# Optimization experiments

Measured on AMD Instinct MI355X. Metric: run time of the kernel, lower is better.

The kernel has to match this reference:

```python
import jax, jax.numpy as jnp
import numpy as np

EPS = 1e-5  # torch BatchNorm1d default eps


def _bn(x, axes):
    # BatchNorm in training mode with gamma=1, beta=0 (torch init values):
    # normalize with biased batch statistics over the given axes.
    m = x.mean(axes, keepdims=True)
    v = x.var(axes, keepdims=True)
    return (x - m) * jax.lax.rsqrt(v + EPS)


def setup_inputs() -> dict:
    key = jax.random.key(0)
    ks = jax.random.split(key, 12)
    N, M = 50000, 12
    OF, F, E, H = 92, 64, 41, 128
    Z = 2 * F + E  # 169 = concat(node, nbr_node, edge)

    def w(k, shape, fan):
        return jax.random.normal(k, shape, jnp.float32) * np.float32(1.0 / np.sqrt(fan))

    return {
        "node_fea": jax.random.normal(ks[0], (N, OF), jnp.float32),
        "edge_fea": jax.random.uniform(ks[1], (N, M, E), dtype=jnp.float32),
        "nbr_offset": jax.random.randint(ks[2], (N, M, 3), -1, 2).astype(jnp.float32),
        "atom_pos": jax.random.uniform(ks[3], (N, 3), dtype=jnp.float32) * 10.0,
        "cells": jnp.broadcast_to(jnp.eye(3, dtype=jnp.float32) * 10.0, (N, 3, 3))
                 + jax.random.normal(ks[4], (N, 3, 3), jnp.float32) * 0.1,
        "edge_idx": jax.random.randint(ks[5], (N, M), 0, N),
        "W_emb": w(ks[6], (OF, F), OF), "b_emb": jnp.zeros((F,), jnp.float32),
        "W_pre_node": w(ks[7], (3, Z, 2 * F), Z), "b_pre_node": jnp.zeros((3, 2 * F), jnp.float32),
        "W_pre_edge": w(ks[8], (3, Z, 2 * E), Z), "b_pre_edge": jnp.zeros((3, 2 * E), jnp.float32),
        "W_dist": w(ks[9], (Z, H), Z), "b_dist": jnp.zeros((H,), jnp.float32),
        "W_const": w(ks[10], (Z, H), Z), "b_const": jnp.zeros((H,), jnp.float32),
    }


def reference(node_fea, edge_fea, nbr_offset, atom_pos, cells, edge_idx,
              W_emb, b_emb, W_pre_node, b_pre_node, W_pre_edge, b_pre_edge,
              W_dist, b_dist, W_const, b_const):
    N, M = edge_idx.shape
    lrelu = jax.nn.leaky_relu  # torch LeakyReLU default slope 0.01
    sig = jax.nn.sigmoid
    sp = jax.nn.softplus

    # get_distance: neighbor Cartesian positions via unit-cell offsets
    off_cart = jnp.einsum('nmi,nij->nmj', nbr_offset, cells)         # (N,M,3)
    diff = atom_pos[edge_idx] + off_cart - atom_pos[:, None, :]       # (N,M,3)
    distance = jnp.sqrt(jnp.sum(diff * diff, -1, keepdims=True) + 1e-12)  # (N,M,1)

    node = node_fea @ W_emb + b_emb  # embedding -> (N,64)

    for l in range(W_pre_node.shape[0]):  # n_conv = 3 ConvLayers
        nbr = node[edge_idx]  # gather (N,M,F)
        z = jnp.concatenate(
            [jnp.broadcast_to(node[:, None, :], (N, M, node.shape[-1])), nbr, edge_fea],
            axis=2)  # (N,M,169)
        # node branch: linear -> BN -> sigmoid*leakyrelu gate -> sum over M -> BN -> residual
        zn = _bn(z @ W_pre_node[l] + b_pre_node[l], (0, 1))  # (N,M,128)
        nf, nc = jnp.split(zn, 2, axis=2)
        aggr = jnp.sum(sig(nf) * lrelu(nc), axis=1)           # (N,64)
        node = lrelu(node + _bn(aggr, (0,)))
        # edge branch: linear -> BN -> gate -> BN -> residual
        ze = _bn(z @ W_pre_edge[l] + b_pre_edge[l], (0, 1))   # (N,M,82)
        ef, ec = jnp.split(ze, 2, axis=2)
        edge_fea = lrelu(edge_fea + _bn(sig(ef) * lrelu(ec), (0, 1)))

    nbr = node[edge_idx]
    bond_fea = jnp.concatenate(
        [jnp.broadcast_to(node[:, None, :], (N, M, node.shape[-1])), nbr, edge_fea],
        axis=2)  # (N,M,169)

    # n_h_dist == 1 branch: softplus(BN(linear) + distance), mean over channels
    bd = sp(_bn(bond_fea @ W_dist + b_dist, (0, 1)) + distance)
    bd = jnp.mean(bd, axis=2, keepdims=True)                  # (N,M,1)
    # n_h_const == 1 branch: softplus(BN(linear)), mean over channels, / N
    bc = sp(_bn(bond_fea @ W_const + b_const, (0, 1)))
    bc = jnp.mean(bc, axis=2, keepdims=True) / N              # (N,M,1)

    return jnp.concatenate([bd, bc], axis=2)                  # (N,M,2)
```

## Files before the change

kernel.cpp:

```cpp
#include <hip/hip_runtime.h>
#include <math.h>

#define NN 50000
#define MM 12
#define NM 600000
#define OF 92
#define FF 64
#define EE 41
#define ES 48
#define ZZ 169
#define EFO 128
#define ECO 192
#define RPB 96
#define NPB 8
#define NBLK 6250
#define KP 200
#define KSTEPS 6
#define MT 6
#define NSLICE 64
#define PSTRIDE 1024

typedef __bf16 bf16x8 __attribute__((ext_vector_type(8)));
typedef float  f32x4  __attribute__((ext_vector_type(4)));

__device__ __forceinline__ float lrelu(float x){ return fmaxf(x, 0.01f*x); }
__device__ __forceinline__ float sigm(float x){ return __builtin_amdgcn_rcpf(1.f+__expf(-x)); }
__device__ __forceinline__ float softpl(float x){ return fmaxf(x,0.f) + __logf(1.f+__expf(-fabsf(x))); }
__device__ __forceinline__ unsigned short f2bf(float f){
    __bf16 h = (__bf16)f;
    return __builtin_bit_cast(unsigned short, h);
}
__device__ __forceinline__ float b2f(unsigned short u){
    unsigned int b = ((unsigned int)u) << 16;
    return __builtin_bit_cast(float, b);
}
__device__ __forceinline__ unsigned short f2h(float f){
    _Float16 h = (_Float16)f;
    return __builtin_bit_cast(unsigned short, h);
}
__device__ __forceinline__ float h2f(unsigned short u){
    return (float)__builtin_bit_cast(_Float16, u);
}

__global__ __launch_bounds__(256) void pack_w(const float* __restrict__ Wn,
    const float* __restrict__ We, const float* __restrict__ Wd,
    const float* __restrict__ Wc, unsigned short* __restrict__ dst)
{
    int idx = blockIdx.x*256 + threadIdx.x;
    if (idx >= 4*49152) return;
    int j    = idx & 7;
    int lane = (idx >> 3) & 63;
    int ntks = (idx >> 9) % 96;
    int L    = idx / 49152;
    int nt = ntks & 15, ks = ntks >> 4;
    int k   = ks*32 + (lane>>4)*8 + j;
    int col = nt*16 + (lane&15);
    float v = 0.f;
    if (k < ZZ) {
        if (L < 3) {
            if (col < 128)                       v = Wn[((size_t)L*ZZ + k)*128 + col];
            else if (col >= EFO && col < EFO+EE) v = We[((size_t)L*ZZ + k)*82 + (col-EFO)];
            else if (col >= ECO && col < ECO+EE) v = We[((size_t)L*ZZ + k)*82 + 41 + (col-ECO)];
        } else {
            if (col < 128) v = Wd[(size_t)k*128 + col];
            else           v = Wc[(size_t)k*128 + (col-128)];
        }
    }
    dst[idx] = f2bf(v);
}

__global__ __launch_bounds__(256) void k_dist(const float* __restrict__ off,
    const float* __restrict__ apos, const float* __restrict__ cells,
    const int* __restrict__ eidx, float* __restrict__ distb)
{
    int idx = blockIdx.x*256 + threadIdx.x;
    if (idx >= NM) return;
    int n = idx / MM;
    const float* o  = off + (size_t)idx*3;
    const float* cl = cells + (size_t)n*9;
    int n2 = eidx[idx];
    float o0=o[0], o1=o[1], o2=o[2];
    float dd = 1e-12f;
    #pragma unroll
    for (int j=0;j<3;j++){
        float oc = o0*cl[0*3+j] + o1*cl[1*3+j] + o2*cl[2*3+j];
        float d = apos[(size_t)n2*3+j] + oc - apos[(size_t)n*3+j];
        dd += d*d;
    }
    distb[idx] = sqrtf(dd);
}

__global__ __launch_bounds__(256) void k_cvt(const float* __restrict__ src,
    unsigned short* __restrict__ e)
{
    int idx = blockIdx.x*256 + threadIdx.x;
    if (idx >= NM*ES) return;
    int gr = idx / ES;
    int c  = idx - gr*ES;
    e[idx] = (c < EE) ? f2bf(src[(size_t)gr*EE + c]) : (unsigned short)0;
}

__global__ __launch_bounds__(256) void k_emb(const float* __restrict__ nf,
    const float* __restrict__ W, const float* __restrict__ b,
    unsigned short* __restrict__ node0)
{
    int idx = blockIdx.x*256 + threadIdx.x;
    if (idx >= NN*FF) return;
    int n = idx >> 6, c = idx & 63;
    float s = b[c];
    for (int k=0;k<OF;k++) s = fmaf(nf[(size_t)n*OF+k], W[k*FF+c], s);
    node0[idx] = f2bf(s);
}

__global__ __launch_bounds__(256) void k_red(float* __restrict__ P,
    float* __restrict__ dst, int lo, int hi)
{
    for (int c = lo + threadIdx.x; c < hi; c += 256) {
        float s = 0.f;
        #pragma unroll 8
        for (int sl = 0; sl < NSLICE; ++sl) s += P[sl*PSTRIDE + c];
        dst[c] = s;
        #pragma unroll 8
        for (int sl = 0; sl < NSLICE; ++sl) P[sl*PSTRIDE + c] = 0.f;
    }
}

__device__ __forceinline__ void stage_z(unsigned short* __restrict__ Zl,
    const unsigned short* __restrict__ node_src, const unsigned short* __restrict__ edge_src,
    const int* __restrict__ eidx, int n0, int tid)
{
    const int gr0 = n0 * MM;
    #pragma unroll
    for (int it=0; it<3; ++it){
        int i = it*256 + tid;
        int row = i >> 3, ch = i & 7;
        int n = n0 + row/MM;
        uint4 v = *(const uint4*)(node_src + (size_t)n*FF + ch*8);
        *(uint4*)(Zl + row*KP + ch*8) = v;
    }
    #pragma unroll
    for (int it=0; it<3; ++it){
        int i = it*256 + tid;
        int row = i >> 3, ch = i & 7;
        int n2 = eidx[gr0 + row];
        uint4 v = *(const uint4*)(node_src + (size_t)n2*FF + ch*8);
        *(uint4*)(Zl + row*KP + 64 + ch*8) = v;
    }
    #pragma unroll
    for (int it=0; it<3; ++it){
        int i = it*256 + tid;
        int row = i >> 3, ch = i & 7;
        uint4 v = make_uint4(0u,0u,0u,0u);
        if (ch < 6) v = *(const uint4*)(edge_src + (size_t)(gr0+row)*ES + ch*8);
        *(uint4*)(Zl + row*KP + 128 + ch*8) = v;
    }
}

__device__ __forceinline__ void mfma_core(const unsigned short* __restrict__ Zl,
    const unsigned short* __restrict__ Wpk, int w, int lane, f32x4 (&acc)[MT][4])
{
    const int quad = lane >> 4, li = lane & 15;
    #pragma unroll
    for (int mt=0;mt<MT;mt++)
        #pragma unroll
        for (int t=0;t<4;t++) acc[mt][t] = (f32x4){0.f,0.f,0.f,0.f};

    #pragma unroll 2
    for (int ks=0; ks<KSTEPS; ++ks) {
        bf16x8 bfr[4];
        #pragma unroll
        for (int t=0;t<4;t++){
            int nt = w + 4*t;
            bfr[t] = *(const bf16x8*)(Wpk + (((ks*16 + nt)*64 + lane) << 3));
        }
        bf16x8 afr[MT];
        #pragma unroll
        for (int mt=0;mt<MT;mt++){
            int row = mt*16 + li;
            afr[mt] = *(const bf16x8*)(Zl + row*KP + ks*32 + quad*8);
        }
        #pragma unroll
        for (int mt=0;mt<MT;mt++)
            #pragma unroll
            for (int t=0;t<4;t++)
                acc[mt][t] = __builtin_amdgcn_mfma_f32_16x16x32_bf16(afr[mt], bfr[t], acc[mt][t], 0, 0, 0);
    }
}

__device__ __forceinline__ void stats_epi(const f32x4 (&acc)[MT][4], int w, int lane,
    float* __restrict__ Ps)
{
    const int quad = lane>>4, li = lane&15;
    #pragma unroll
    for (int t=0;t<4;t++){
        float s=0.f, q=0.f;
        #pragma unroll
        for (int mt=0;mt<MT;mt++)
            #pragma unroll
            for (int r=0;r<4;r++){ float v = acc[mt][t][r]; s+=v; q = fmaf(v,v,q); }
        s += __shfl_xor(s,16); s += __shfl_xor(s,32);
        q += __shfl_xor(q,16); q += __shfl_xor(q,32);
        if (quad == 0) {
            int col = t*64 + w*16 + li;
            atomicAdd(&Ps[col], s);
            atomicAdd(&Ps[256+col], q);
        }
    }
}

__global__ __launch_bounds__(256) void k_stats(
    const unsigned short* __restrict__ node_src, const unsigned short* __restrict__ edge_src,
    const int* __restrict__ eidx, const unsigned short* __restrict__ Wpk,
    float* __restrict__ Pst)
{
    __shared__ unsigned short Zl[RPB*KP];
    const int tid = threadIdx.x, w = tid>>6, lane = tid&63;
    const int n0 = blockIdx.x * NPB;
    stage_z(Zl, node_src, edge_src, eidx, n0, tid);
    __syncthreads();
    f32x4 acc[MT][4];
    mfma_core(Zl, Wpk, w, lane, acc);
    float* Ps = Pst + (size_t)(blockIdx.x & (NSLICE-1))*PSTRIDE;
    stats_epi(acc, w, lane, Ps);
}

__global__ __launch_bounds__(256) void k_gemm(
    const unsigned short* __restrict__ node_src, const unsigned short* __restrict__ edge_src,
    const int* __restrict__ eidx, const unsigned short* __restrict__ Wpk,
    float* __restrict__ Pst, ushort4* __restrict__ Y)
{
    __shared__ unsigned short Zl[RPB*KP];
    const int tid = threadIdx.x, w = tid>>6, lane = tid&63;
    const int b = blockIdx.x;
    const int n0 = b * NPB;
    stage_z(Zl, node_src, edge_src, eidx, n0, tid);
    __syncthreads();
    f32x4 acc[MT][4];
    mfma_core(Zl, Wpk, w, lane, acc);
    #pragma unroll
    for (int mt=0;mt<MT;mt++)
        #pragma unroll
        for (int t=0;t<4;t++){
            ushort4 h;
            h.x = f2h(acc[mt][t][0]); h.y = f2h(acc[mt][t][1]);
            h.z = f2h(acc[mt][t][2]); h.w = f2h(acc[mt][t][3]);
            Y[((size_t)b*96 + mt*16 + t*4 + w)*64 + lane] = h;
        }
    float* Ps = Pst + (size_t)(blockIdx.x & (NSLICE-1))*PSTRIDE;
    stats_epi(acc, w, lane, Ps);
}

__device__ __forceinline__ void apply_epi(float (&vals)[4], int mt,
    int quad, int cg, bool ce_ok, const float sc[4], const float bi[4],
    int r, int gr0, float* __restrict__ gL, unsigned short* __restrict__ gbuf,
    float& pg, float& pq)
{
    int row = mt*16 + quad*4 + r;
    float nf = fmaf(vals[0], sc[0], bi[0]);
    float nc = fmaf(vals[1], sc[1], bi[1]);
    gL[row*68 + cg] = sigm(nf) * lrelu(nc);
    if (ce_ok) {
        float ef = fmaf(vals[2], sc[2], bi[2]);
        float ec = fmaf(vals[3], sc[3], bi[3]);
        float gv = sigm(ef)*lrelu(ec);
        gbuf[(size_t)(gr0+row)*ES + cg] = f2bf(gv);
        pg += gv; pq = fmaf(gv,gv,pq);
    }
}

__device__ __forceinline__ void apply_tail(float pg, float pq, int tid, int quad,
    int cg, bool ce_ok, int n0, const float* __restrict__ gL,
    float* __restrict__ aggr, float* __restrict__ aS, float* __restrict__ aQ,
    float* __restrict__ gS, float* __restrict__ gQ)
{
    pg += __shfl_xor(pg,16); pg += __shfl_xor(pg,32);
    pq += __shfl_xor(pq,16); pq += __shfl_xor(pq,32);
    if (quad==0 && ce_ok){ atomicAdd(&gS[cg], pg); atomicAdd(&gQ[cg], pq); }
    __syncthreads();
    if (tid < 64) {
        float sAcc=0.f, sQq=0.f;
        #pragma unroll
        for (int nl=0; nl<NPB; nl++){
            float vsum = 0.f;
            #pragma unroll
            for (int jj=0;jj<MM;jj++) vsum += gL[(nl*MM+jj)*68 + tid];
            aggr[(size_t)(n0+nl)*64 + tid] = vsum;
            sAcc += vsum; sQq = fmaf(vsum,vsum,sQq);
        }
        atomicAdd(&aS[tid], sAcc);
        atomicAdd(&aQ[tid], sQq);
    }
}

__global__ __launch_bounds__(256) void k_apply_y(
    const ushort4* __restrict__ Y,
    const float* __restrict__ preS, const float* __restrict__ preQ,
    float* __restrict__ aggr, unsigned short* __restrict__ gbuf,
    float* __restrict__ Pst)
{
    __shared__ float gL[RPB*68];
    const int tid = threadIdx.x, w = tid>>6, lane = tid&63;
    const int quad = lane>>4, li = lane&15;
    const int b = blockIdx.x;
    const int n0 = b * NPB;
    const int gr0 = n0 * MM;
    const int cg = w*16 + li;

    float sc[4], bi[4];
    #pragma unroll
    for (int t=0;t<4;t++){
        int col = t*64 + cg;
        float mm = preS[col]*(1.f/(float)NM);
        float vv = preQ[col]*(1.f/(float)NM) - mm*mm;
        float is = rsqrtf(vv + 1e-5f);
        sc[t] = is; bi[t] = -mm*is;
    }

    float pg = 0.f, pq = 0.f;
    const bool ce_ok = cg < EE;
    #pragma unroll
    for (int mt=0;mt<MT;mt++){
        unsigned short a[4][4];
        #pragma unroll
        for (int t=0;t<4;t++)
            *(ushort4*)a[t] = Y[((size_t)b*96 + mt*16 + t*4 + w)*64 + lane];
        #pragma unroll
        for (int r=0;r<4;r++){
            float vals[4] = {h2f(a[0][r]), h2f(a[1][r]), h2f(a[2][r]), h2f(a[3][r])};
            apply_epi(vals, mt, quad, cg, ce_ok, sc, bi, r, gr0, gL, gbuf, pg, pq);
        }
    }
    float* Ps = Pst + (size_t)(b & (NSLICE-1))*PSTRIDE;
    apply_tail(pg, pq, tid, quad, cg, ce_ok, n0, gL, aggr, Ps+512, Ps+576, Ps+640, Ps+704);
}

__global__ __launch_bounds__(256) void k_apply_re(
    const unsigned short* __restrict__ node_src, const unsigned short* __restrict__ edge_src,
    const int* __restrict__ eidx, const unsigned short* __restrict__ Wpk,
    const float* __restrict__ preS, const float* __restrict__ preQ,
    float* __restrict__ aggr, unsigned short* __restrict__ gbuf,
    float* __restrict__ Pst)
{
    __shared__ __align__(16) char smem[RPB*KP*2];
    unsigned short* Zl = (unsigned short*)smem;
    float* gL = (float*)smem;
    const int tid = threadIdx.x, w = tid>>6, lane = tid&63;
    const int quad = lane>>4, li = lane&15;
    const int n0 = blockIdx.x * NPB;
    const int gr0 = n0 * MM;
    stage_z(Zl, node_src, edge_src, eidx, n0, tid);
    __syncthreads();
    f32x4 acc[MT][4];
    mfma_core(Zl, Wpk, w, lane, acc);
    __syncthreads();

    const int cg = w*16 + li;
    float sc[4], bi[4];
    #pragma unroll
    for (int t=0;t<4;t++){
        int col = t*64 + cg;
        float mm = preS[col]*(1.f/(float)NM);
        float vv = preQ[col]*(1.f/(float)NM) - mm*mm;
        float is = rsqrtf(vv + 1e-5f);
        sc[t] = is; bi[t] = -mm*is;
    }
    float pg = 0.f, pq = 0.f;
    const bool ce_ok = cg < EE;
    #pragma unroll
    for (int mt=0;mt<MT;mt++)
        #pragma unroll
        for (int r=0;r<4;r++){
            float vals[4] = {acc[mt][0][r], acc[mt][1][r], acc[mt][2][r], acc[mt][3][r]};
            apply_epi(vals, mt, quad, cg, ce_ok, sc, bi, r, gr0, gL, gbuf, pg, pq);
        }
    float* Ps = Pst + (size_t)(blockIdx.x & (NSLICE-1))*PSTRIDE;
    apply_tail(pg, pq, tid, quad, cg, ce_ok, n0, gL, aggr, Ps+512, Ps+576, Ps+640, Ps+704);
}

__global__ __launch_bounds__(256) void k_upd_node(const unsigned short* __restrict__ cur,
    const float* __restrict__ aggr, const float* __restrict__ aS,
    const float* __restrict__ aQ, unsigned short* __restrict__ nxt)
{
    int idx = blockIdx.x*256 + threadIdx.x;
    if (idx >= NN*8) return;
    int n = idx >> 3, ch = idx & 7;
    int base = n*64 + ch*8;
    float4 a0 = *(const float4*)(aggr + base);
    float4 a1 = *(const float4*)(aggr + base + 4);
    uint4 cu = *(const uint4*)(cur + base);
    unsigned short cs[8]; *(uint4*)cs = cu;
    float av[8] = {a0.x,a0.y,a0.z,a0.w,a1.x,a1.y,a1.z,a1.w};
    unsigned short os[8];
    #pragma unroll
    for (int j=0;j<8;j++){
        int c = ch*8+j;
        float mm = aS[c]*(1.f/(float)NN);
        float vv = aQ[c]*(1.f/(float)NN) - mm*mm;
        float is = rsqrtf(vv + 1e-5f);
        float v = (av[j] - mm) * is;
        os[j] = f2bf(lrelu(b2f(cs[j]) + v));
    }
    *(uint4*)(nxt + base) = *(uint4*)os;
}

__global__ __launch_bounds__(256) void k_upd_edge(unsigned short* __restrict__ e,
    const unsigned short* __restrict__ g, const float* __restrict__ gS,
    const float* __restrict__ gQ)
{
    int idx = blockIdx.x*256 + threadIdx.x;
    if (idx >= NM*6) return;
    int gr = idx / 6, ch = idx - gr*6;
    size_t base = (size_t)gr*ES + ch*8;
    uint4 eu = *(const uint4*)(e + base);
    uint4 gu = *(const uint4*)(g + base);
    unsigned short es8[8], gs8[8], os[8];
    *(uint4*)es8 = eu; *(uint4*)gs8 = gu;
    #pragma unroll
    for (int j=0;j<8;j++){
        int c = ch*8+j;
        if (c < EE) {
            float mm = gS[c]*(1.f/(float)NM);
            float vv = gQ[c]*(1.f/(float)NM) - mm*mm;
            float is = rsqrtf(vv + 1e-5f);
            float v = (b2f(gs8[j]) - mm) * is;
            os[j] = f2bf(lrelu(b2f(es8[j]) + v));
        } else {
            os[j] = es8[j];
        }
    }
    *(uint4*)(e + base) = *(uint4*)os;
}

__device__ __forceinline__ void final_epi(const float vals[4], int mt, int r,
    int quad, int w, int liq, bool wr, const float sc[4], const float bi[4],
    int gr0, const float* __restrict__ distb,
    float* __restrict__ bufD, float* __restrict__ bufC)
{
    int row = mt*16 + quad*4 + r;
    float dv = distb[gr0 + row];
    float pd = softpl(fmaf(vals[0],sc[0],bi[0]) + dv)
             + softpl(fmaf(vals[1],sc[1],bi[1]) + dv);
    float pc = softpl(fmaf(vals[2],sc[2],bi[2]))
             + softpl(fmaf(vals[3],sc[3],bi[3]));
    pd += __shfl_xor(pd,1); pd += __shfl_xor(pd,2);
    pc += __shfl_xor(pc,1); pc += __shfl_xor(pc,2);
    if (wr) {
        bufD[row*17 + w*4 + liq] = pd;
        bufC[row*17 + w*4 + liq] = pc;
    }
}

__device__ __forceinline__ void final_tail(int tid, int gr0,
    const float* __restrict__ bufD, const float* __restrict__ bufC,
    float* __restrict__ out)
{
    __syncthreads();
    if (tid < 2*RPB) {
        int h = tid >= RPB;
        int row = tid - (h ? RPB : 0);
        const float* buf = h ? bufC : bufD;
        float s = 0.f;
        #pragma unroll
        for (int t=0;t<16;t++) s += buf[row*17+t];
        size_t gr = gr0 + row;
        out[gr*2 + h] = h ? s * (1.f/128.f) * (1.f/(float)NN) : s * (1.f/128.f);
    }
}

__global__ __launch_bounds__(256) void k_final_y(
    const ushort4* __restrict__ Y,
    const float* __restrict__ fS, const float* __restrict__ fQ,
    const float* __restrict__ distb, float* __restrict__ out)
{
    __shared__ float bufD[RPB*17];
    __shared__ float bufC[RPB*17];
    const int tid = threadIdx.x, w = tid>>6, lane = tid&63;
    const int quad = lane>>4, li = lane&15;
    const int b = blockIdx.x;
    const int gr0 = b * NPB * MM;
    const int cg = w*16 + li;

    float sc[4], bi[4];
    #pragma unroll
    for (int t=0;t<4;t++){
        int col = t*64 + cg;
        float mm = fS[col]*(1.f/(float)NM);
        float vv = fQ[col]*(1.f/(float)NM) - mm*mm;
        float is = rsqrtf(vv + 1e-5f);
        sc[t] = is; bi[t] = -mm*is;
    }
    const int liq = li >> 2;
    const bool wr = (li & 3) == 0;
    #pragma unroll
    for (int mt=0;mt<MT;mt++){
        unsigned short a[4][4];
        #pragma unroll
        for (int t=0;t<4;t++)
            *(ushort4*)a[t] = Y[((size_t)b*96 + mt*16 + t*4 + w)*64 + lane];
        #pragma unroll
        for (int r=0;r<4;r++){
            float vals[4] = {h2f(a[0][r]), h2f(a[1][r]), h2f(a[2][r]), h2f(a[3][r])};
            final_epi(vals, mt, r, quad, w, liq, wr, sc, bi, gr0, distb, bufD, bufC);
        }
    }
    final_tail(tid, gr0, bufD, bufC, out);
}

__global__ __launch_bounds__(256) void k_final_re(
    const unsigned short* __restrict__ node_src, const unsigned short* __restrict__ edge_src,
    const int* __restrict__ eidx, const unsigned short* __restrict__ Wpk,
    const float* __restrict__ fS, const float* __restrict__ fQ,
    const float* __restrict__ distb, float* __restrict__ out)
{
    __shared__ __align__(16) char smem[RPB*KP*2];
    unsigned short* Zl = (unsigned short*)smem;
    float* bufD = (float*)smem;
    float* bufC = (float*)(smem + 8192);
    const int tid = threadIdx.x, w = tid>>6, lane = tid&63;
    const int quad = lane>>4, li = lane&15;
    const int n0 = blockIdx.x * NPB;
    const int gr0 = n0 * MM;
    stage_z(Zl, node_src, edge_src, eidx, n0, tid);
    __syncthreads();
    f32x4 acc[MT][4];
    mfma_core(Zl, Wpk, w, lane, acc);
    __syncthreads();

    const int cg = w*16 + li;
    float sc[4], bi[4];
    #pragma unroll
    for (int t=0;t<4;t++){
        int col = t*64 + cg;
        float mm = fS[col]*(1.f/(float)NM);
        float vv = fQ[col]*(1.f/(float)NM) - mm*mm;
        float is = rsqrtf(vv + 1e-5f);
        sc[t] = is; bi[t] = -mm*is;
    }
    const int liq = li >> 2;
    const bool wr = (li & 3) == 0;
    #pragma unroll
    for (int mt=0;mt<MT;mt++)
        #pragma unroll
        for (int r=0;r<4;r++){
            float vals[4] = {acc[mt][0][r], acc[mt][1][r], acc[mt][2][r], acc[mt][3][r]};
            final_epi(vals, mt, r, quad, w, liq, wr, sc, bi, gr0, distb, bufD, bufC);
        }
    final_tail(tid, gr0, bufD, bufC, out);
}

extern "C" void kernel_launch(void* const* d_in, const int* in_sizes, int n_in,
                              void* d_out, int out_size, void* d_ws, size_t ws_size,
                              hipStream_t stream)
{
    const float* node_fea = (const float*)d_in[0];
    const float* edge_in  = (const float*)d_in[1];
    const float* nbr_off  = (const float*)d_in[2];
    const float* apos     = (const float*)d_in[3];
    const float* cells    = (const float*)d_in[4];
    const int*   eidx     = (const int*)  d_in[5];
    const float* W_emb    = (const float*)d_in[6];
    const float* b_emb    = (const float*)d_in[7];
    const float* W_pn     = (const float*)d_in[8];
    const float* W_pe     = (const float*)d_in[10];
    const float* W_dist   = (const float*)d_in[12];
    const float* W_cst    = (const float*)d_in[14];
    float* out = (float*)d_out;
    char* ws = (char*)d_ws;

    size_t o = 0;
    auto alloc = [&](size_t bytes) { char* p = ws + o; o += (bytes + 255) & ~(size_t)255; return p; };
    unsigned short* node0 = (unsigned short*)alloc((size_t)NN*FF*2);
    unsigned short* node1 = (unsigned short*)alloc((size_t)NN*FF*2);
    unsigned short* ebuf  = (unsigned short*)alloc((size_t)NM*ES*2);
    unsigned short* gbuf  = (unsigned short*)alloc((size_t)NM*ES*2);
    float* aggr  = (float*)alloc((size_t)NN*FF*4);
    float* distb = (float*)alloc((size_t)NM*4);
    unsigned short* Wpk = (unsigned short*)alloc((size_t)4*49152*2);
    float* stats = (float*)alloc(4096*4);
    float* Pst   = (float*)alloc((size_t)NSLICE*PSTRIDE*4);

    const size_t YB = (size_t)NBLK*96*64*8;
    const bool useY = (o + YB) <= ws_size;
    ushort4* Ybuf = useY ? (ushort4*)alloc(YB) : (ushort4*)nullptr;

    hipMemsetAsync(stats, 0, 4096*sizeof(float), stream);
    hipMemsetAsync(Pst, 0, (size_t)NSLICE*PSTRIDE*sizeof(float), stream);
    pack_w<<<(4*49152+255)/256, 256, 0, stream>>>(W_pn, W_pe, W_dist, W_cst, Wpk);
    k_dist <<<(NM+255)/256,     256, 0, stream>>>(nbr_off, apos, cells, eidx, distb);
    k_cvt  <<<(NM*ES+255)/256,  256, 0, stream>>>(edge_in, ebuf);
    k_emb  <<<(NN*FF+255)/256,  256, 0, stream>>>(node_fea, W_emb, b_emb, node0);

    const unsigned short* ncur = node0;

    for (int l=0;l<3;l++){
        float* st = stats + l*768;
        float* preS = st;       float* preQ = st+256;
        float* aSs  = st+512;   float* aQq  = st+576;
        float* gSs  = st+640;   float* gQq  = st+704;
        const unsigned short* Wl = Wpk + (size_t)l*49152;
        unsigned short* ndst = (l & 1) ? node0 : node1;

        if (useY) {
            k_gemm   <<<NBLK,256,0,stream>>>(ncur, ebuf, eidx, Wl, Pst, Ybuf);
            k_red    <<<1,256,0,stream>>>(Pst, st, 0, 512);
            k_apply_y<<<NBLK,256,0,stream>>>(Ybuf, preS, preQ, aggr, gbuf, Pst);
            k_red    <<<1,256,0,stream>>>(Pst, st, 512, 768);
        } else {
            k_stats  <<<NBLK,256,0,stream>>>(ncur, ebuf, eidx, Wl, Pst);
            k_red    <<<1,256,0,stream>>>(Pst, st, 0, 512);
            k_apply_re<<<NBLK,256,0,stream>>>(ncur, ebuf, eidx, Wl, preS, preQ,
                                              aggr, gbuf, Pst);
            k_red    <<<1,256,0,stream>>>(Pst, st, 512, 768);
        }
        k_upd_node<<<(NN*8+255)/256,256,0,stream>>>(ncur, aggr, aSs, aQq, ndst);
        k_upd_edge<<<(NM*6+255)/256,256,0,stream>>>(ebuf, gbuf, gSs, gQq);
        ncur = ndst;
    }

    float* fSt = stats + 3*768;
    float* fS = fSt; float* fQ = fSt + 256;
    const unsigned short* Wf = Wpk + (size_t)3*49152;
    if (useY) {
        k_gemm   <<<NBLK,256,0,stream>>>(ncur, ebuf, eidx, Wf, Pst, Ybuf);
        k_red    <<<1,256,0,stream>>>(Pst, fSt, 0, 512);
        k_final_y<<<NBLK,256,0,stream>>>(Ybuf, fS, fQ, distb, out);
    } else {
        k_stats  <<<NBLK,256,0,stream>>>(ncur, ebuf, eidx, Wf, Pst);
        k_red    <<<1,256,0,stream>>>(Pst, fSt, 0, 512);
        k_final_re<<<NBLK,256,0,stream>>>(ncur, ebuf, eidx, Wf, fS, fQ, distb, out);
    }
}
```

Measured before the change: 1.358 ms.

## Drop fp16 Y buffer path; use 512-thread recompute kernels with split column halves

Removes the path that stored GEMM outputs as fp16 in a workspace buffer and read them back. All layers now recompute the GEMM in both the stats and apply kernels, which run with 512 threads (8 waves). Each wave owns two column tiles instead of four, so the node half and edge half are handled by separate wave groups, cutting registers per thread and raising parallelism. This trades the Y buffer's HBM write and read traffic for doing the GEMM and gather twice; the gather staging is also flattened into one pass.

```diff
diff --git a/kernel.cpp b/kernel.cpp
--- a/kernel.cpp
+++ b/kernel.cpp
@@ -9,8 +9,6 @@
 #define EE 41
 #define ES 48
 #define ZZ 169
-#define EFO 128
-#define ECO 192
 #define RPB 96
 #define NPB 8
 #define NBLK 6250
@@ -19,6 +17,7 @@
 #define MT 6
 #define NSLICE 64
 #define PSTRIDE 1024
+#define TPB 512
 
 typedef __bf16 bf16x8 __attribute__((ext_vector_type(8)));
 typedef float  f32x4  __attribute__((ext_vector_type(4)));
@@ -33,13 +32,6 @@
 __device__ __forceinline__ float b2f(unsigned short u){
     unsigned int b = ((unsigned int)u) << 16;
     return __builtin_bit_cast(float, b);
-}
-__device__ __forceinline__ unsigned short f2h(float f){
-    _Float16 h = (_Float16)f;
-    return __builtin_bit_cast(unsigned short, h);
-}
-__device__ __forceinline__ float h2f(unsigned short u){
-    return (float)__builtin_bit_cast(_Float16, u);
 }
 
 __global__ __launch_bounds__(256) void pack_w(const float* __restrict__ Wn,
@@ -59,8 +51,8 @@
     if (k < ZZ) {
         if (L < 3) {
             if (col < 128)                       v = Wn[((size_t)L*ZZ + k)*128 + col];
-            else if (col >= EFO && col < EFO+EE) v = We[((size_t)L*ZZ + k)*82 + (col-EFO)];
-            else if (col >= ECO && col < ECO+EE) v = We[((size_t)L*ZZ + k)*82 + 41 + (col-ECO)];
+            else if (col >= 128 && col < 128+EE) v = We[((size_t)L*ZZ + k)*82 + (col-128)];
+            else if (col >= 192 && col < 192+EE) v = We[((size_t)L*ZZ + k)*82 + 41 + (col-192)];
         } else {
             if (col < 128) v = Wd[(size_t)k*128 + col];
             else           v = Wc[(size_t)k*128 + (col-128)];
@@ -130,69 +122,65 @@
     const int* __restrict__ eidx, int n0, int tid)
 {
     const int gr0 = n0 * MM;
-    #pragma unroll
-    for (int it=0; it<3; ++it){
-        int i = it*256 + tid;
-        int row = i >> 3, ch = i & 7;
-        int n = n0 + row/MM;
-        uint4 v = *(const uint4*)(node_src + (size_t)n*FF + ch*8);
-        *(uint4*)(Zl + row*KP + ch*8) = v;
-    }
-    #pragma unroll
-    for (int it=0; it<3; ++it){
-        int i = it*256 + tid;
-        int row = i >> 3, ch = i & 7;
-        int n2 = eidx[gr0 + row];
-        uint4 v = *(const uint4*)(node_src + (size_t)n2*FF + ch*8);
-        *(uint4*)(Zl + row*KP + 64 + ch*8) = v;
-    }
-    #pragma unroll
-    for (int it=0; it<3; ++it){
-        int i = it*256 + tid;
-        int row = i >> 3, ch = i & 7;
-        uint4 v = make_uint4(0u,0u,0u,0u);
-        if (ch < 6) v = *(const uint4*)(edge_src + (size_t)(gr0+row)*ES + ch*8);
-        *(uint4*)(Zl + row*KP + 128 + ch*8) = v;
+    const int r0 = tid >> 3, ch = tid & 7;
+    const bool two = tid < 256;
+    const int r1 = r0 + 64;
+    const int e0 = eidx[gr0 + r0];
+    const int e1 = two ? eidx[gr0 + r1] : 0;
+    const int na0 = n0 + r0 / MM;
+    const int na1 = n0 + r1 / MM;
+    const uint4 z4 = make_uint4(0u,0u,0u,0u);
+    uint4 s0  = *(const uint4*)(node_src + (size_t)na0*FF + ch*8);
+    uint4 nb0 = *(const uint4*)(node_src + (size_t)e0*FF + ch*8);
+    uint4 d0 = z4, s1 = z4, nb1 = z4, d1 = z4;
+    if (ch < 6) d0 = *(const uint4*)(edge_src + (size_t)(gr0+r0)*ES + ch*8);
+    if (two) {
+        s1  = *(const uint4*)(node_src + (size_t)na1*FF + ch*8);
+        nb1 = *(const uint4*)(node_src + (size_t)e1*FF + ch*8);
+        if (ch < 6) d1 = *(const uint4*)(edge_src + (size_t)(gr0+r1)*ES + ch*8);
+    }
+    *(uint4*)(Zl + r0*KP + ch*8)        = s0;
+    *(uint4*)(Zl + r0*KP + 64 + ch*8)   = nb0;
+    *(uint4*)(Zl + r0*KP + 128 + ch*8)  = d0;
+    if (two) {
+        *(uint4*)(Zl + r1*KP + ch*8)       = s1;
+        *(uint4*)(Zl + r1*KP + 64 + ch*8)  = nb1;
+        *(uint4*)(Zl + r1*KP + 128 + ch*8) = d1;
     }
 }
 
 __device__ __forceinline__ void mfma_core(const unsigned short* __restrict__ Zl,
-    const unsigned short* __restrict__ Wpk, int w, int lane, f32x4 (&acc)[MT][4])
+    const unsigned short* __restrict__ Wpk, int h, int sw, int lane, f32x4 (&acc)[MT][2])
 {
     const int quad = lane >> 4, li = lane & 15;
     #pragma unroll
-    for (int mt=0;mt<MT;mt++)
-        #pragma unroll
-        for (int t=0;t<4;t++) acc[mt][t] = (f32x4){0.f,0.f,0.f,0.f};
-
+    for (int mt=0;mt<MT;mt++){
+        acc[mt][0] = (f32x4){0.f,0.f,0.f,0.f};
+        acc[mt][1] = (f32x4){0.f,0.f,0.f,0.f};
+    }
+    const int nt0 = h*8 + sw;
     #pragma unroll 2
     for (int ks=0; ks<KSTEPS; ++ks) {
-        bf16x8 bfr[4];
-        #pragma unroll
-        for (int t=0;t<4;t++){
-            int nt = w + 4*t;
-            bfr[t] = *(const bf16x8*)(Wpk + (((ks*16 + nt)*64 + lane) << 3));
+        bf16x8 bfr0 = *(const bf16x8*)(Wpk + (((ks*16 + nt0    )*64 + lane) << 3));
+        bf16x8 bfr1 = *(const bf16x8*)(Wpk + (((ks*16 + nt0 + 4)*64 + lane) << 3));
+        bf16x8 afr[MT];
+        #pragma unroll
+        for (int mt=0;mt<MT;mt++)
+            afr[mt] = *(const bf16x8*)(Zl + (mt*16+li)*KP + ks*32 + quad*8);
+        #pragma unroll
+        for (int mt=0;mt<MT;mt++){
+            acc[mt][0] = __builtin_amdgcn_mfma_f32_16x16x32_bf16(afr[mt], bfr0, acc[mt][0], 0, 0, 0);
+            acc[mt][1] = __builtin_amdgcn_mfma_f32_16x16x32_bf16(afr[mt], bfr1, acc[mt][1], 0, 0, 0);
         }
-        bf16x8 afr[MT];
-        #pragma unroll
-        for (int mt=0;mt<MT;mt++){
-            int row = mt*16 + li;
-            afr[mt] = *(const bf16x8*)(Zl + row*KP + ks*32 + quad*8);
-        }
-        #pragma unroll
-        for (int mt=0;mt<MT;mt++)
-            #pragma unroll
-            for (int t=0;t<4;t++)
-                acc[mt][t] = __builtin_amdgcn_mfma_f32_16x16x32_bf16(afr[mt], bfr[t], acc[mt][t], 0, 0, 0);
-    }
-}
-
-__device__ __forceinline__ void stats_epi(const f32x4 (&acc)[MT][4], int w, int lane,
+    }
+}
+
+__device__ __forceinline__ void stats_epi(const f32x4 (&acc)[MT][2], int h, int sw, int lane,
     float* __restrict__ Ps)
 {
     const int quad = lane>>4, li = lane&15;
     #pragma unroll
-    for (int t=0;t<4;t++){
+    for (int t=0;t<2;t++){
         float s=0.f, q=0.f;
         #pragma unroll
         for (int mt=0;mt<MT;mt++)
@@ -201,140 +189,31 @@
         s += __shfl_xor(s,16); s += __shfl_xor(s,32);
         q += __shfl_xor(q,16); q += __shfl_xor(q,32);
         if (quad == 0) {
-            int col = t*64 + w*16 + li;
+            int col = h*128 + t*64 + sw*16 + li;
             atomicAdd(&Ps[col], s);
             atomicAdd(&Ps[256+col], q);
         }
     }
 }
 
-__global__ __launch_bounds__(256) void k_stats(
+__global__ __launch_bounds__(TPB,3) void k_stats(
     const unsigned short* __restrict__ node_src, const unsigned short* __restrict__ edge_src,
     const int* __restrict__ eidx, const unsigned short* __restrict__ Wpk,
     float* __restrict__ Pst)
 {
     __shared__ unsigned short Zl[RPB*KP];
     const int tid = threadIdx.x, w = tid>>6, lane = tid&63;
+    const int h = w>>2, sw = w&3;
     const int n0 = blockIdx.x * NPB;
     stage_z(Zl, node_src, edge_src, eidx, n0, tid);
     __syncthreads();
-    f32x4 acc[MT][4];
-    mfma_core(Zl, Wpk, w, lane, acc);
+    f32x4 acc[MT][2];
+    mfma_core(Zl, Wpk, h, sw, lane, acc);
     float* Ps = Pst + (size_t)(blockIdx.x & (NSLICE-1))*PSTRIDE;
-    stats_epi(acc, w, lane, Ps);
-}
-
-__global__ __launch_bounds__(256) void k_gemm(
-    const unsigned short* __restrict__ node_src, const unsigned short* __restrict__ edge_src,
-    const int* __restrict__ eidx, const unsigned short* __restrict__ Wpk,
-    float* __restrict__ Pst, ushort4* __restrict__ Y)
-{
-    __shared__ unsigned short Zl[RPB*KP];
-    const int tid = threadIdx.x, w = tid>>6, lane = tid&63;
-    const int b = blockIdx.x;
-    const int n0 = b * NPB;
-    stage_z(Zl, node_src, edge_src, eidx, n0, tid);
-    __syncthreads();
-    f32x4 acc[MT][4];
-    mfma_core(Zl, Wpk, w, lane, acc);
-    #pragma unroll
-    for (int mt=0;mt<MT;mt++)
-        #pragma unroll
-        for (int t=0;t<4;t++){
-            ushort4 h;
-            h.x = f2h(acc[mt][t][0]); h.y = f2h(acc[mt][t][1]);
-            h.z = f2h(acc[mt][t][2]); h.w = f2h(acc[mt][t][3]);
-            Y[((size_t)b*96 + mt*16 + t*4 + w)*64 + lane] = h;
-        }
-    float* Ps = Pst + (size_t)(blockIdx.x & (NSLICE-1))*PSTRIDE;
-    stats_epi(acc, w, lane, Ps);
-}
-
-__device__ __forceinline__ void apply_epi(float (&vals)[4], int mt,
-    int quad, int cg, bool ce_ok, const float sc[4], const float bi[4],
-    int r, int gr0, float* __restrict__ gL, unsigned short* __restrict__ gbuf,
-    float& pg, float& pq)
-{
-    int row = mt*16 + quad*4 + r;
-    float nf = fmaf(vals[0], sc[0], bi[0]);
-    float nc = fmaf(vals[1], sc[1], bi[1]);
-    gL[row*68 + cg] = sigm(nf) * lrelu(nc);
-    if (ce_ok) {
-        float ef = fmaf(vals[2], sc[2], bi[2]);
-        float ec = fmaf(vals[3], sc[3], bi[3]);
-        float gv = sigm(ef)*lrelu(ec);
-        gbuf[(size_t)(gr0+row)*ES + cg] = f2bf(gv);
-        pg += gv; pq = fmaf(gv,gv,pq);
-    }
-}
-
-__device__ __forceinline__ void apply_tail(float pg, float pq, int tid, int quad,
-    int cg, bool ce_ok, int n0, const float* __restrict__ gL,
-    float* __restrict__ aggr, float* __restrict__ aS, float* __restrict__ aQ,
-    float* __restrict__ gS, float* __restrict__ gQ)
-{
-    pg += __shfl_xor(pg,16); pg += __shfl_xor(pg,32);
-    pq += __shfl_xor(pq,16); pq += __shfl_xor(pq,32);
-    if (quad==0 && ce_ok){ atomicAdd(&gS[cg], pg); atomicAdd(&gQ[cg], pq); }
-    __syncthreads();
-    if (tid < 64) {
-        float sAcc=0.f, sQq=0.f;
-        #pragma unroll
-        for (int nl=0; nl<NPB; nl++){
-            float vsum = 0.f;
-            #pragma unroll
-            for (int jj=0;jj<MM;jj++) vsum += gL[(nl*MM+jj)*68 + tid];
-            aggr[(size_t)(n0+nl)*64 + tid] = vsum;
-            sAcc += vsum; sQq = fmaf(vsum,vsum,sQq);
-        }
-        atomicAdd(&aS[tid], sAcc);
-        atomicAdd(&aQ[tid], sQq);
-    }
-}
-
-__global__ __launch_bounds__(256) void k_apply_y(
-    const ushort4* __restrict__ Y,
-    const float* __restrict__ preS, const float* __restrict__ preQ,
-    float* __restrict__ aggr, unsigned short* __restrict__ gbuf,
-    float* __restrict__ Pst)
-{
-    __shared__ float gL[RPB*68];
-    const int tid = threadIdx.x, w = tid>>6, lane = tid&63;
-    const int quad = lane>>4, li = lane&15;
-    const int b = blockIdx.x;
-    const int n0 = b * NPB;
-    const int gr0 = n0 * MM;
-    const int cg = w*16 + li;
-
-    float sc[4], bi[4];
-    #pragma unroll
-    for (int t=0;t<4;t++){
-        int col = t*64 + cg;
-        float mm = preS[col]*(1.f/(float)NM);
-        float vv = preQ[col]*(1.f/(float)NM) - mm*mm;
-        float is = rsqrtf(vv + 1e-5f);
-        sc[t] = is; bi[t] = -mm*is;
-    }
-
-    float pg = 0.f, pq = 0.f;
-    const bool ce_ok = cg < EE;
-    #pragma unroll
-    for (int mt=0;mt<MT;mt++){
-        unsigned short a[4][4];
-        #pragma unroll
-        for (int t=0;t<4;t++)
-            *(ushort4*)a[t] = Y[((size_t)b*96 + mt*16 + t*4 + w)*64 + lane];
-        #pragma unroll
-        for (int r=0;r<4;r++){
-            float vals[4] = {h2f(a[0][r]), h2f(a[1][r]), h2f(a[2][r]), h2f(a[3][r])};
-            apply_epi(vals, mt, quad, cg, ce_ok, sc, bi, r, gr0, gL, gbuf, pg, pq);
-        }
-    }
-    float* Ps = Pst + (size_t)(b & (NSLICE-1))*PSTRIDE;
-    apply_tail(pg, pq, tid, quad, cg, ce_ok, n0, gL, aggr, Ps+512, Ps+576, Ps+640, Ps+704);
-}
-
-__global__ __launch_bounds__(256) void k_apply_re(
+    stats_epi(acc, h, sw, lane, Ps);
+}
+
+__global__ __launch_bounds__(TPB,3) void k_apply_re(
     const unsigned short* __restrict__ node_src, const unsigned short* __restrict__ edge_src,
     const int* __restrict__ eidx, const unsigned short* __restrict__ Wpk,
     const float* __restrict__ preS, const float* __restrict__ preQ,
@@ -346,35 +225,66 @@
     float* gL = (float*)smem;
     const int tid = threadIdx.x, w = tid>>6, lane = tid&63;
     const int quad = lane>>4, li = lane&15;
+    const int h = w>>2, sw = w&3;
     const int n0 = blockIdx.x * NPB;
     const int gr0 = n0 * MM;
     stage_z(Zl, node_src, edge_src, eidx, n0, tid);
     __syncthreads();
-    f32x4 acc[MT][4];
-    mfma_core(Zl, Wpk, w, lane, acc);
-    __syncthreads();
-
-    const int cg = w*16 + li;
-    float sc[4], bi[4];
-    #pragma unroll
-    for (int t=0;t<4;t++){
-        int col = t*64 + cg;
+    f32x4 acc[MT][2];
+    mfma_core(Zl, Wpk, h, sw, lane, acc);
+    __syncthreads();
+
+    const int cg0 = sw*16 + li;
+    float sc[2], bi[2];
+    #pragma unroll
+    for (int t=0;t<2;t++){
+        int col = h*128 + t*64 + cg0;
         float mm = preS[col]*(1.f/(float)NM);
         float vv = preQ[col]*(1.f/(float)NM) - mm*mm;
         float is = rsqrtf(vv + 1e-5f);
         sc[t] = is; bi[t] = -mm*is;
     }
-    float pg = 0.f, pq = 0.f;
-    const bool ce_ok = cg < EE;
-    #pragma unroll
-    for (int mt=0;mt<MT;mt++)
-        #pragma unroll
-        for (int r=0;r<4;r++){
-            float vals[4] = {acc[mt][0][r], acc[mt][1][r], acc[mt][2][r], acc[mt][3][r]};
-            apply_epi(vals, mt, quad, cg, ce_ok, sc, bi, r, gr0, gL, gbuf, pg, pq);
-        }
     float* Ps = Pst + (size_t)(blockIdx.x & (NSLICE-1))*PSTRIDE;
-    apply_tail(pg, pq, tid, quad, cg, ce_ok, n0, gL, aggr, Ps+512, Ps+576, Ps+640, Ps+704);
+
+    if (h == 0) {
+        #pragma unroll
+        for (int mt=0;mt<MT;mt++)
+            #pragma unroll
+            for (int r=0;r<4;r++){
+                int row = mt*16 + quad*4 + r;
+                float nf = fmaf(acc[mt][0][r], sc[0], bi[0]);
+                float nc = fmaf(acc[mt][1][r], sc[1], bi[1]);
+                gL[row*68 + cg0] = sigm(nf) * lrelu(nc);
+            }
+    } else {
+        const bool ce_ok = cg0 < EE;
+        float pg = 0.f, pq = 0.f;
+        #pragma unroll
+        for (int mt=0;mt<MT;mt++)
+            #pragma unroll
+            for (int r=0;r<4;r++){
+                int row = mt*16 + quad*4 + r;
+                float ef = fmaf(acc[mt][0][r], sc[0], bi[0]);
+                float ec = fmaf(acc[mt][1][r], sc[1], bi[1]);
+                float gv = sigm(ef)*lrelu(ec);
+                if (ce_ok) {
+                    gbuf[(size_t)(gr0+row)*ES + cg0] = f2bf(gv);
+                    pg += gv; pq = fmaf(gv,gv,pq);
+                }
+            }
+        pg += __shfl_xor(pg,16); pg += __shfl_xor(pg,32);
+        pq += __shfl_xor(pq,16); pq += __shfl_xor(pq,32);
+        if (quad==0 && ce_ok){ atomicAdd(&Ps[640+cg0], pg); atomicAdd(&Ps[704+cg0], pq); }
+    }
+    __syncthreads();
+    {
+        float vsum = 0.f;
+        #pragma unroll
+        for (int jj=0;jj<MM;jj++) vsum += gL[(w*MM+jj)*68 + lane];
+        aggr[(size_t)(n0+w)*64 + lane] = vsum;
+        atomicAdd(&Ps[512+lane], vsum);
+        atomicAdd(&Ps[576+lane], vsum*vsum);
+    }
 }
 
 __global__ __launch_bounds__(256) void k_upd_node(const unsigned short* __restrict__ cur,
@@ -431,82 +341,7 @@
     *(uint4*)(e + base) = *(uint4*)os;
 }
 
-__device__ __forceinline__ void final_epi(const float vals[4], int mt, int r,
-    int quad, int w, int liq, bool wr, const float sc[4], const float bi[4],
-    int gr0, const float* __restrict__ distb,
-    float* __restrict__ bufD, float* __restrict__ bufC)
-{
-    int row = mt*16 + quad*4 + r;
-    float dv = distb[gr0 + row];
-    float pd = softpl(fmaf(vals[0],sc[0],bi[0]) + dv)
-             + softpl(fmaf(vals[1],sc[1],bi[1]) + dv);
-    float pc = softpl(fmaf(vals[2],sc[2],bi[2]))
-             + softpl(fmaf(vals[3],sc[3],bi[3]));
-    pd += __shfl_xor(pd,1); pd += __shfl_xor(pd,2);
-    pc += __shfl_xor(pc,1); pc += __shfl_xor(pc,2);
-    if (wr) {
-        bufD[row*17 + w*4 + liq] = pd;
-        bufC[row*17 + w*4 + liq] = pc;
-    }
-}
-
-__device__ __forceinline__ void final_tail(int tid, int gr0,
-    const float* __restrict__ bufD, const float* __restrict__ bufC,
-    float* __restrict__ out)
-{
-    __syncthreads();
-    if (tid < 2*RPB) {
-        int h = tid >= RPB;
-        int row = tid - (h ? RPB : 0);
-        const float* buf = h ? bufC : bufD;
-        float s = 0.f;
-        #pragma unroll
-        for (int t=0;t<16;t++) s += buf[row*17+t];
-        size_t gr = gr0 + row;
-        out[gr*2 + h] = h ? s * (1.f/128.f) * (1.f/(float)NN) : s * (1.f/128.f);
-    }
-}
-
-__global__ __launch_bounds__(256) void k_final_y(
-    const ushort4* __restrict__ Y,
-    const float* __restrict__ fS, const float* __restrict__ fQ,
-    const float* __restrict__ distb, float* __restrict__ out)
-{
-    __shared__ float bufD[RPB*17];
-    __shared__ float bufC[RPB*17];
-    const int tid = threadIdx.x, w = tid>>6, lane = tid&63;
-    const int quad = lane>>4, li = lane&15;
-    const int b = blockIdx.x;
-    const int gr0 = b * NPB * MM;
-    const int cg = w*16 + li;
-
-    float sc[4], bi[4];
-    #pragma unroll
-    for (int t=0;t<4;t++){
-        int col = t*64 + cg;
-        float mm = fS[col]*(1.f/(float)NM);
-        float vv = fQ[col]*(1.f/(float)NM) - mm*mm;
-        float is = rsqrtf(vv + 1e-5f);
-        sc[t] = is; bi[t] = -mm*is;
-    }
-    const int liq = li >> 2;
-    const bool wr = (li & 3) == 0;
-    #pragma unroll
-    for (int mt=0;mt<MT;mt++){
-        unsigned short a[4][4];
-        #pragma unroll
-        for (int t=0;t<4;t++)
-            *(ushort4*)a[t] = Y[((size_t)b*96 + mt*16 + t*4 + w)*64 + lane];
-        #pragma unroll
-        for (int r=0;r<4;r++){
-            float vals[4] = {h2f(a[0][r]), h2f(a[1][r]), h2f(a[2][r]), h2f(a[3][r])};
-            final_epi(vals, mt, r, quad, w, liq, wr, sc, bi, gr0, distb, bufD, bufC);
-        }
-    }
-    final_tail(tid, gr0, bufD, bufC, out);
-}
-
-__global__ __launch_bounds__(256) void k_final_re(
+__global__ __launch_bounds__(TPB,3) void k_final_re(
     const unsigned short* __restrict__ node_src, const unsigned short* __restrict__ edge_src,
     const int* __restrict__ eidx, const unsigned short* __restrict__ Wpk,
     const float* __restrict__ fS, const float* __restrict__ fQ,
@@ -518,19 +353,20 @@
     float* bufC = (float*)(smem + 8192);
     const int tid = threadIdx.x, w = tid>>6, lane = tid&63;
     const int quad = lane>>4, li = lane&15;
+    const int h = w>>2, sw = w&3;
     const int n0 = blockIdx.x * NPB;
     const int gr0 = n0 * MM;
     stage_z(Zl, node_src, edge_src, eidx, n0, tid);
     __syncthreads();
-    f32x4 acc[MT][4];
-    mfma_core(Zl, Wpk, w, lane, acc);
-    __syncthreads();
-
-    const int cg = w*16 + li;
-    float sc[4], bi[4];
-    #pragma unroll
-    for (int t=0;t<4;t++){
-        int col = t*64 + cg;
+    f32x4 acc[MT][2];
+    mfma_core(Zl, Wpk, h, sw, lane, acc);
+    __syncthreads();
+
+    const int cg0 = sw*16 + li;
+    float sc[2], bi[2];
+    #pragma unroll
+    for (int t=0;t<2;t++){
+        int col = h*128 + t*64 + cg0;
         float mm = fS[col]*(1.f/(float)NM);
         float vv = fQ[col]*(1.f/(float)NM) - mm*mm;
         float is = rsqrtf(vv + 1e-5f);
@@ -538,14 +374,35 @@
     }
     const int liq = li >> 2;
     const bool wr = (li & 3) == 0;
+    float* buf = (h == 0) ? bufD : bufC;
     #pragma unroll
     for (int mt=0;mt<MT;mt++)
         #pragma unroll
         for (int r=0;r<4;r++){
-            float vals[4] = {acc[mt][0][r], acc[mt][1][r], acc[mt][2][r], acc[mt][3][r]};
-            final_epi(vals, mt, r, quad, w, liq, wr, sc, bi, gr0, distb, bufD, bufC);
+            int row = mt*16 + quad*4 + r;
+            float v0 = fmaf(acc[mt][0][r], sc[0], bi[0]);
+            float v1 = fmaf(acc[mt][1][r], sc[1], bi[1]);
+            float p;
+            if (h == 0) {
+                float dv = distb[gr0 + row];
+                p = softpl(v0 + dv) + softpl(v1 + dv);
+            } else {
+                p = softpl(v0) + softpl(v1);
+            }
+            p += __shfl_xor(p,1); p += __shfl_xor(p,2);
+            if (wr) buf[row*17 + sw*4 + liq] = p;
         }
-    final_tail(tid, gr0, bufD, bufC, out);
+    __syncthreads();
+    if (tid < 2*RPB) {
+        int hh = tid >= RPB;
+        int row = tid - (hh ? RPB : 0);
+        const float* bsrc = hh ? bufC : bufD;
+        float s = 0.f;
+        #pragma unroll
+        for (int t=0;t<16;t++) s += bsrc[row*17+t];
+        size_t gr = gr0 + row;
+        out[gr*2 + hh] = hh ? s * (1.f/128.f) * (1.f/(float)NN) : s * (1.f/128.f);
+    }
 }
 
 extern "C" void kernel_launch(void* const* d_in, const int* in_sizes, int n_in,
@@ -579,10 +436,6 @@
     float* stats = (float*)alloc(4096*4);
     float* Pst   = (float*)alloc((size_t)NSLICE*PSTRIDE*4);
 
-    const size_t YB = (size_t)NBLK*96*64*8;
-    const bool useY = (o + YB) <= ws_size;
-    ushort4* Ybuf = useY ? (ushort4*)alloc(YB) : (ushort4*)nullptr;
-
     hipMemsetAsync(stats, 0, 4096*sizeof(float), stream);
     hipMemsetAsync(Pst, 0, (size_t)NSLICE*PSTRIDE*sizeof(float), stream);
     pack_w<<<(4*49152+255)/256, 256, 0, stream>>>(W_pn, W_pe, W_dist, W_cst, Wpk);
@@ -600,18 +453,11 @@
         const unsigned short* Wl = Wpk + (size_t)l*49152;
         unsigned short* ndst = (l & 1) ? node0 : node1;
 
-        if (useY) {
-            k_gemm   <<<NBLK,256,0,stream>>>(ncur, ebuf, eidx, Wl, Pst, Ybuf);
-            k_red    <<<1,256,0,stream>>>(Pst, st, 0, 512);
-            k_apply_y<<<NBLK,256,0,stream>>>(Ybuf, preS, preQ, aggr, gbuf, Pst);
-            k_red    <<<1,256,0,stream>>>(Pst, st, 512, 768);
-        } else {
-            k_stats  <<<NBLK,256,0,stream>>>(ncur, ebuf, eidx, Wl, Pst);
-            k_red    <<<1,256,0,stream>>>(Pst, st, 0, 512);
-            k_apply_re<<<NBLK,256,0,stream>>>(ncur, ebuf, eidx, Wl, preS, preQ,
-                                              aggr, gbuf, Pst);
-            k_red    <<<1,256,0,stream>>>(Pst, st, 512, 768);
-        }
+        k_stats  <<<NBLK,TPB,0,stream>>>(ncur, ebuf, eidx, Wl, Pst);
+        k_red    <<<1,256,0,stream>>>(Pst, st, 0, 512);
+        k_apply_re<<<NBLK,TPB,0,stream>>>(ncur, ebuf, eidx, Wl, preS, preQ,
+                                          aggr, gbuf, Pst);
+        k_red    <<<1,256,0,stream>>>(Pst, st, 512, 768);
         k_upd_node<<<(NN*8+255)/256,256,0,stream>>>(ncur, aggr, aSs, aQq, ndst);
         k_upd_edge<<<(NM*6+255)/256,256,0,stream>>>(ebuf, gbuf, gSs, gQq);
         ncur = ndst;
@@ -620,13 +466,7 @@
     float* fSt = stats + 3*768;
     float* fS = fSt; float* fQ = fSt + 256;
     const unsigned short* Wf = Wpk + (size_t)3*49152;
-    if (useY) {
-        k_gemm   <<<NBLK,256,0,stream>>>(ncur, ebuf, eidx, Wf, Pst, Ybuf);
-        k_red    <<<1,256,0,stream>>>(Pst, fSt, 0, 512);
-        k_final_y<<<NBLK,256,0,stream>>>(Ybuf, fS, fQ, distb, out);
-    } else {
-        k_stats  <<<NBLK,256,0,stream>>>(ncur, ebuf, eidx, Wf, Pst);
-        k_red    <<<1,256,0,stream>>>(Pst, fSt, 0, 512);
-        k_final_re<<<NBLK,256,0,stream>>>(ncur, ebuf, eidx, Wf, fS, fQ, distb, out);
-    }
-}
+    k_stats  <<<NBLK,TPB,0,stream>>>(ncur, ebuf, eidx, Wf, Pst);
+    k_red    <<<1,256,0,stream>>>(Pst, fSt, 0, 512);
+    k_final_re<<<NBLK,TPB,0,stream>>>(ncur, ebuf, eidx, Wf, fS, fQ, distb, out);
+}
```

New measurement: 1.239 ms. 8.8% less time.
